# Optimization experiments

Measured on AMD Instinct MI355X. Metric: run time of the kernel, lower is better.

Reference implementation:

```python
import jax, jax.numpy as jnp
import numpy as np

HIDDEN = 4096
NUM_EXPERTS = 64
TOP_K = 2
N_TOKENS = 16384


def setup_inputs() -> dict:
    key = jax.random.key(0)
    kx, kw = jax.random.split(key)
    x = jax.random.normal(kx, (N_TOKENS, HIDDEN), dtype=jnp.float32)
    # nn.Linear(hidden, num_experts, bias=False) weight: [num_experts, hidden]
    gate_w = jax.random.normal(kw, (NUM_EXPERTS, HIDDEN), dtype=jnp.float32) * (HIDDEN ** -0.5)
    return {"x": x, "gate_w": gate_w}


def reference(x, gate_w):
    # logits: [N, num_experts]
    logits = jnp.einsum("nh,eh->ne", x, gate_w)
    topk_vals, topk_idx = jax.lax.top_k(logits, TOP_K)  # [N, k]
    topk_gates = jax.nn.softmax(topk_vals, axis=-1)
    return topk_gates, topk_idx
```

## Files before the change

kernel.cpp:

```cpp
#include <hip/hip_runtime.h>

#define NTOK 16384
#define HID  4096
#define NEXP 64
#define BM   64
#define BK   64
#define NSTEPS (HID / BK)

typedef _Float16 f16;
typedef f16  f16x4 __attribute__((ext_vector_type(4)));
typedef f16  f16x8 __attribute__((ext_vector_type(8)));
typedef float f32x4 __attribute__((ext_vector_type(4)));

__device__ __forceinline__ int swz_base(int row, int unit) {
    return row * 64 + ((unit ^ (row & 7)) << 3);
}

__global__ __launch_bounds__(512)
void topk_gate_kernel(const float* __restrict__ x,
                      const float* __restrict__ w,
                      float* __restrict__ out) {
    __shared__ __align__(16) f16 Ah[BM * BK];
    __shared__ __align__(16) f16 Al[BM * BK];
    __shared__ __align__(16) f16 Bh[NEXP * BK];
    __shared__ __align__(16) f16 Bl[NEXP * BK];
    __shared__ float red[2][BM][4];

    const int t    = threadIdx.x;
    const int blk  = blockIdx.x;
    const int lane = t & 63;
    const int wid  = t >> 6;
    const int wm   = wid & 3;
    const int wn   = wid >> 2;

    const bool isB   = (t >= 256);
    const int  tt    = t & 255;
    const int  srow  = tt >> 2;
    const int  sq    = (tt & 3) * 4;
    const float scale = isB ? 64.0f : 1.0f;
    const float* src = isB ? (w + (size_t)srow * HID + sq * 4)
                           : (x + ((size_t)blk * BM + srow) * HID + sq * 4);
    f16* dstH = isB ? Bh : Ah;
    f16* dstL = isB ? Bl : Al;

    f32x4 acc0 = {0.f, 0.f, 0.f, 0.f};
    f32x4 acc1 = {0.f, 0.f, 0.f, 0.f};

    const int col = lane & 15;
    const int grp = lane >> 4;

    float4 cur[4];
    #pragma unroll
    for (int i = 0; i < 4; ++i)
        cur[i] = *(const float4*)(src + 0 * BK + i * 4);

    for (int s = 0; s < NSTEPS; ++s) {
        const int sn = (s + 1 < NSTEPS) ? (s + 1) : s;
        float4 nxt[4];
        #pragma unroll
        for (int i = 0; i < 4; ++i)
            nxt[i] = *(const float4*)(src + (size_t)sn * BK + i * 4);

        __syncthreads();

        #pragma unroll
        for (int i = 0; i < 4; ++i) {
            float4 v = cur[i];
            float sx = v.x * scale, sy = v.y * scale, sz = v.z * scale, sw = v.w * scale;
            f16 hx = (f16)sx, hy = (f16)sy, hz = (f16)sz, hw = (f16)sw;
            f16 lx = (f16)(sx - (float)hx);
            f16 ly = (f16)(sy - (float)hy);
            f16 lz = (f16)(sz - (float)hz);
            f16 lw = (f16)(sw - (float)hw);
            int q   = sq + i;
            int off = swz_base(srow, q >> 1) + (q & 1) * 4;
            *(f16x4*)&dstH[off] = (f16x4){hx, hy, hz, hw};
            *(f16x4*)&dstL[off] = (f16x4){lx, ly, lz, lw};
        }
        __syncthreads();

        const int arow  = wm * 16 + col;
        const int brow0 = wn * 32 + col;
        const int brow1 = brow0 + 16;
        #pragma unroll
        for (int s2 = 0; s2 < 2; ++s2) {
            int u = s2 * 4 + grp;
            f16x8 ah  = *(const f16x8*)&Ah[swz_base(arow,  u)];
            f16x8 al  = *(const f16x8*)&Al[swz_base(arow,  u)];
            f16x8 b0h = *(const f16x8*)&Bh[swz_base(brow0, u)];
            f16x8 b0l = *(const f16x8*)&Bl[swz_base(brow0, u)];
            f16x8 b1h = *(const f16x8*)&Bh[swz_base(brow1, u)];
            f16x8 b1l = *(const f16x8*)&Bl[swz_base(brow1, u)];
            acc0 = __builtin_amdgcn_mfma_f32_16x16x32_f16(ah, b0h, acc0, 0, 0, 0);
            acc0 = __builtin_amdgcn_mfma_f32_16x16x32_f16(ah, b0l, acc0, 0, 0, 0);
            acc0 = __builtin_amdgcn_mfma_f32_16x16x32_f16(al, b0h, acc0, 0, 0, 0);
            acc1 = __builtin_amdgcn_mfma_f32_16x16x32_f16(ah, b1h, acc1, 0, 0, 0);
            acc1 = __builtin_amdgcn_mfma_f32_16x16x32_f16(ah, b1l, acc1, 0, 0, 0);
            acc1 = __builtin_amdgcn_mfma_f32_16x16x32_f16(al, b1h, acc1, 0, 0, 0);
        }

        #pragma unroll
        for (int i = 0; i < 4; ++i) cur[i] = nxt[i];
    }

    #pragma unroll
    for (int r = 0; r < 4; ++r) {
        float va = acc0[r], vb = acc1[r];
        int   ia = wn * 32 + col, ib = ia + 16;
        float v0, v1; int i0, i1;
        if (va >= vb) { v0 = va; i0 = ia; v1 = vb; i1 = ib; }
        else          { v0 = vb; i0 = ib; v1 = va; i1 = ia; }
        #pragma unroll
        for (int m = 1; m <= 8; m <<= 1) {
            float ov0 = __shfl_xor(v0, m, 64);
            int   oi0 = __shfl_xor(i0, m, 64);
            float ov1 = __shfl_xor(v1, m, 64);
            int   oi1 = __shfl_xor(i1, m, 64);
            bool ob = (ov0 > v0) || (ov0 == v0 && oi0 < i0);
            if (ob) {
                bool k2 = (v0 > ov1) || (v0 == ov1 && i0 < oi1);
                v1 = k2 ? v0 : ov1; i1 = k2 ? i0 : oi1;
                v0 = ov0; i0 = oi0;
            } else {
                bool k2 = (ov0 > v1) || (ov0 == v1 && oi0 < i1);
                v1 = k2 ? ov0 : v1; i1 = k2 ? oi0 : i1;
            }
        }
        if (col == 0) {
            int tl = wm * 16 + grp * 4 + r;
            red[wn][tl][0] = v0; red[wn][tl][1] = (float)i0;
            red[wn][tl][2] = v1; red[wn][tl][3] = (float)i1;
        }
    }
    __syncthreads();

    if (t < BM) {
        float a0 = red[0][t][0]; int ai0 = (int)red[0][t][1];
        float a1 = red[0][t][2]; int ai1 = (int)red[0][t][3];
        float b0 = red[1][t][0]; int bi0 = (int)red[1][t][1];
        float b1 = red[1][t][2]; int bi1 = (int)red[1][t][3];
        float v0, v1; int i0, i1;
        bool bb = (b0 > a0) || (b0 == a0 && bi0 < ai0);
        if (bb) {
            v0 = b0; i0 = bi0;
            bool k2 = (a0 > b1) || (a0 == b1 && ai0 < bi1);
            v1 = k2 ? a0 : b1; i1 = k2 ? ai0 : bi1;
        } else {
            v0 = a0; i0 = ai0;
            bool k2 = (b0 > a1) || (b0 == a1 && bi0 < ai1);
            v1 = k2 ? b0 : a1; i1 = k2 ? bi0 : ai1;
        }
        float d  = (v1 - v0) * (1.0f / 64.0f);
        float e  = expf(d);
        float g0 = 1.0f / (1.0f + e);
        float g1 = e / (1.0f + e);

        int tok = blk * BM + t;
        out[(size_t)tok * 2 + 0] = g0;
        out[(size_t)tok * 2 + 1] = g1;
        out[(size_t)NTOK * 2 + (size_t)tok * 2 + 0] = (float)i0;
        out[(size_t)NTOK * 2 + (size_t)tok * 2 + 1] = (float)i1;
    }
}

extern "C" void kernel_launch(void* const* d_in, const int* in_sizes, int n_in,
                              void* d_out, int out_size, void* d_ws, size_t ws_size,
                              hipStream_t stream) {
    const float* x = (const float*)d_in[0];
    const float* w = (const float*)d_in[1];
    float* out = (float*)d_out;
    (void)in_sizes; (void)n_in; (void)out_size; (void)d_ws; (void)ws_size;

    dim3 grid(NTOK / BM);
    dim3 block(512);
    topk_gate_kernel<<<grid, block, 0, stream>>>(x, w, out);
}
```

Before: 64.25 us.

## Prepack gate weights into MFMA fragment layout and double-buffer x tiles

Adds a pre-pass kernel that converts the gate weights once per call into hi/lo fp16 planes laid out in MFMA B-fragment order inside the workspace. The main kernel then loads B straight from global memory into registers instead of converting it into shared memory in every block and every K step. The token tile drops to 32 rows with 8 waves each owning 16 experts, the x tile is double-buffered in shared memory so there is one barrier per step, and the top-2 merge now runs over four wave groups. The cost is a second kernel launch, and all blocks re-read the packed weights from L2.

```diff
diff --git a/kernel.cpp b/kernel.cpp
--- a/kernel.cpp
+++ b/kernel.cpp
@@ -3,113 +3,128 @@
 #define NTOK 16384
 #define HID  4096
 #define NEXP 64
-#define BM   64
+#define BM   32
 #define BK   64
 #define NSTEPS (HID / BK)
+#define PLANE  (NEXP * HID)
 
 typedef _Float16 f16;
 typedef f16  f16x4 __attribute__((ext_vector_type(4)));
 typedef f16  f16x8 __attribute__((ext_vector_type(8)));
 typedef float f32x4 __attribute__((ext_vector_type(4)));
 
-__device__ __forceinline__ int swz_base(int row, int unit) {
-    return row * 64 + ((unit ^ (row & 7)) << 3);
+__device__ __forceinline__ int swz(int row, int unit16) {
+    return row * 64 + ((unit16 ^ (row & 7)) << 3);
 }
 
-__global__ __launch_bounds__(512)
+__global__ __launch_bounds__(256)
+void pack_w_kernel(const float* __restrict__ w, f16* __restrict__ wp) {
+    int tid = blockIdx.x * 256 + threadIdx.x;
+    int e = tid >> 9;
+    int k = (tid & 511) << 3;
+    const float* src = w + (size_t)e * HID + k;
+    float4 v0 = *(const float4*)(src);
+    float4 v1 = *(const float4*)(src + 4);
+    float sv[8] = {v0.x, v0.y, v0.z, v0.w, v1.x, v1.y, v1.z, v1.w};
+    f16x8 hi, lo;
+    #pragma unroll
+    for (int j = 0; j < 8; ++j) {
+        float s = sv[j] * 64.0f;
+        f16 h = (f16)s;
+        hi[j] = h;
+        lo[j] = (f16)(s - (float)h);
+    }
+    int ks   = k >> 5;
+    int g    = e >> 4;
+    int lane = ((k >> 3) & 3) * 16 + (e & 15);
+    size_t dst = ((size_t)(ks * 4 + g) * 64 + lane) * 8;
+    *(f16x8*)&wp[dst]         = hi;
+    *(f16x8*)&wp[PLANE + dst] = lo;
+}
+
+__global__ __launch_bounds__(512, 4)
 void topk_gate_kernel(const float* __restrict__ x,
-                      const float* __restrict__ w,
+                      const f16* __restrict__ wp,
                       float* __restrict__ out) {
-    __shared__ __align__(16) f16 Ah[BM * BK];
-    __shared__ __align__(16) f16 Al[BM * BK];
-    __shared__ __align__(16) f16 Bh[NEXP * BK];
-    __shared__ __align__(16) f16 Bl[NEXP * BK];
-    __shared__ float red[2][BM][4];
+    __shared__ __align__(16) f16 Ah[2][BM * BK];
+    __shared__ __align__(16) f16 Al[2][BM * BK];
+    __shared__ float red[4][BM][4];
 
     const int t    = threadIdx.x;
     const int blk  = blockIdx.x;
     const int lane = t & 63;
     const int wid  = t >> 6;
-    const int wm   = wid & 3;
-    const int wn   = wid >> 2;
+    const int wm   = wid & 1;
+    const int wn   = wid >> 1;
+    const int col  = lane & 15;
+    const int grp  = lane >> 4;
 
-    const bool isB   = (t >= 256);
-    const int  tt    = t & 255;
-    const int  srow  = tt >> 2;
-    const int  sq    = (tt & 3) * 4;
-    const float scale = isB ? 64.0f : 1.0f;
-    const float* src = isB ? (w + (size_t)srow * HID + sq * 4)
-                           : (x + ((size_t)blk * BM + srow) * HID + sq * 4);
-    f16* dstH = isB ? Bh : Ah;
-    f16* dstL = isB ? Bl : Al;
+    const int srow = t >> 4;
+    const int sq4  = t & 15;
+    const float* asrc = x + ((size_t)blk * BM + srow) * HID + sq4 * 4;
+    const int aoff = swz(srow, sq4 >> 1) + (sq4 & 1) * 4;
 
-    f32x4 acc0 = {0.f, 0.f, 0.f, 0.f};
-    f32x4 acc1 = {0.f, 0.f, 0.f, 0.f};
+    const f16* bp = wp + ((size_t)(wn * 64 + lane)) * 8;
 
-    const int col = lane & 15;
-    const int grp = lane >> 4;
+    f32x4 acc = {0.f, 0.f, 0.f, 0.f};
+    const int arow = wm * 16 + col;
 
-    float4 cur[4];
-    #pragma unroll
-    for (int i = 0; i < 4; ++i)
-        cur[i] = *(const float4*)(src + 0 * BK + i * 4);
+    float4 a_cur = *(const float4*)(asrc);
+    {
+        float4 v = a_cur;
+        f16 hx=(f16)v.x, hy=(f16)v.y, hz=(f16)v.z, hw=(f16)v.w;
+        *(f16x4*)&Ah[0][aoff] = (f16x4){hx,hy,hz,hw};
+        *(f16x4*)&Al[0][aoff] = (f16x4){(f16)(v.x-(float)hx),(f16)(v.y-(float)hy),
+                                        (f16)(v.z-(float)hz),(f16)(v.w-(float)hw)};
+    }
+    float4 a_nxt = *(const float4*)(asrc + BK);
+    f16x8 bh0c = *(const f16x8*)(bp + 0);
+    f16x8 bl0c = *(const f16x8*)(bp + PLANE + 0);
+    f16x8 bh1c = *(const f16x8*)(bp + 2048);
+    f16x8 bl1c = *(const f16x8*)(bp + PLANE + 2048);
+    __syncthreads();
 
     for (int s = 0; s < NSTEPS; ++s) {
+        const int buf = s & 1;
         const int sn = (s + 1 < NSTEPS) ? (s + 1) : s;
-        float4 nxt[4];
-        #pragma unroll
-        for (int i = 0; i < 4; ++i)
-            nxt[i] = *(const float4*)(src + (size_t)sn * BK + i * 4);
+        const size_t bo = (size_t)sn * 4096;
+        f16x8 bh0n = *(const f16x8*)(bp + bo);
+        f16x8 bl0n = *(const f16x8*)(bp + PLANE + bo);
+        f16x8 bh1n = *(const f16x8*)(bp + bo + 2048);
+        f16x8 bl1n = *(const f16x8*)(bp + PLANE + bo + 2048);
+        float4 a_n2 = (s + 2 < NSTEPS) ? *(const float4*)(asrc + (size_t)(s + 2) * BK)
+                                       : a_nxt;
 
-        __syncthreads();
+        {
+            f16x8 ah = *(const f16x8*)&Ah[buf][swz(arow, grp)];
+            f16x8 al = *(const f16x8*)&Al[buf][swz(arow, grp)];
+            acc = __builtin_amdgcn_mfma_f32_16x16x32_f16(ah, bh0c, acc, 0, 0, 0);
+            acc = __builtin_amdgcn_mfma_f32_16x16x32_f16(ah, bl0c, acc, 0, 0, 0);
+            acc = __builtin_amdgcn_mfma_f32_16x16x32_f16(al, bh0c, acc, 0, 0, 0);
+            ah = *(const f16x8*)&Ah[buf][swz(arow, 4 + grp)];
+            al = *(const f16x8*)&Al[buf][swz(arow, 4 + grp)];
+            acc = __builtin_amdgcn_mfma_f32_16x16x32_f16(ah, bh1c, acc, 0, 0, 0);
+            acc = __builtin_amdgcn_mfma_f32_16x16x32_f16(ah, bl1c, acc, 0, 0, 0);
+            acc = __builtin_amdgcn_mfma_f32_16x16x32_f16(al, bh1c, acc, 0, 0, 0);
+        }
 
-        #pragma unroll
-        for (int i = 0; i < 4; ++i) {
-            float4 v = cur[i];
-            float sx = v.x * scale, sy = v.y * scale, sz = v.z * scale, sw = v.w * scale;
-            f16 hx = (f16)sx, hy = (f16)sy, hz = (f16)sz, hw = (f16)sw;
-            f16 lx = (f16)(sx - (float)hx);
-            f16 ly = (f16)(sy - (float)hy);
-            f16 lz = (f16)(sz - (float)hz);
-            f16 lw = (f16)(sw - (float)hw);
-            int q   = sq + i;
-            int off = swz_base(srow, q >> 1) + (q & 1) * 4;
-            *(f16x4*)&dstH[off] = (f16x4){hx, hy, hz, hw};
-            *(f16x4*)&dstL[off] = (f16x4){lx, ly, lz, lw};
+        if (s + 1 < NSTEPS) {
+            float4 v = a_nxt;
+            f16 hx=(f16)v.x, hy=(f16)v.y, hz=(f16)v.z, hw=(f16)v.w;
+            *(f16x4*)&Ah[buf ^ 1][aoff] = (f16x4){hx,hy,hz,hw};
+            *(f16x4*)&Al[buf ^ 1][aoff] = (f16x4){(f16)(v.x-(float)hx),(f16)(v.y-(float)hy),
+                                                  (f16)(v.z-(float)hz),(f16)(v.w-(float)hw)};
         }
         __syncthreads();
 
-        const int arow  = wm * 16 + col;
-        const int brow0 = wn * 32 + col;
-        const int brow1 = brow0 + 16;
-        #pragma unroll
-        for (int s2 = 0; s2 < 2; ++s2) {
-            int u = s2 * 4 + grp;
-            f16x8 ah  = *(const f16x8*)&Ah[swz_base(arow,  u)];
-            f16x8 al  = *(const f16x8*)&Al[swz_base(arow,  u)];
-            f16x8 b0h = *(const f16x8*)&Bh[swz_base(brow0, u)];
-            f16x8 b0l = *(const f16x8*)&Bl[swz_base(brow0, u)];
-            f16x8 b1h = *(const f16x8*)&Bh[swz_base(brow1, u)];
-            f16x8 b1l = *(const f16x8*)&Bl[swz_base(brow1, u)];
-            acc0 = __builtin_amdgcn_mfma_f32_16x16x32_f16(ah, b0h, acc0, 0, 0, 0);
-            acc0 = __builtin_amdgcn_mfma_f32_16x16x32_f16(ah, b0l, acc0, 0, 0, 0);
-            acc0 = __builtin_amdgcn_mfma_f32_16x16x32_f16(al, b0h, acc0, 0, 0, 0);
-            acc1 = __builtin_amdgcn_mfma_f32_16x16x32_f16(ah, b1h, acc1, 0, 0, 0);
-            acc1 = __builtin_amdgcn_mfma_f32_16x16x32_f16(ah, b1l, acc1, 0, 0, 0);
-            acc1 = __builtin_amdgcn_mfma_f32_16x16x32_f16(al, b1h, acc1, 0, 0, 0);
-        }
-
-        #pragma unroll
-        for (int i = 0; i < 4; ++i) cur[i] = nxt[i];
+        a_nxt = a_n2;
+        bh0c = bh0n; bl0c = bl0n; bh1c = bh1n; bl1c = bl1n;
     }
 
     #pragma unroll
     for (int r = 0; r < 4; ++r) {
-        float va = acc0[r], vb = acc1[r];
-        int   ia = wn * 32 + col, ib = ia + 16;
-        float v0, v1; int i0, i1;
-        if (va >= vb) { v0 = va; i0 = ia; v1 = vb; i1 = ib; }
-        else          { v0 = vb; i0 = ib; v1 = va; i1 = ia; }
+        float v0 = acc[r]; int i0 = wn * 16 + col;
+        float v1 = -INFINITY; int i1 = 0x7fffffff;
         #pragma unroll
         for (int m = 1; m <= 8; m <<= 1) {
             float ov0 = __shfl_xor(v0, m, 64);
@@ -135,20 +150,21 @@
     __syncthreads();
 
     if (t < BM) {
-        float a0 = red[0][t][0]; int ai0 = (int)red[0][t][1];
-        float a1 = red[0][t][2]; int ai1 = (int)red[0][t][3];
-        float b0 = red[1][t][0]; int bi0 = (int)red[1][t][1];
-        float b1 = red[1][t][2]; int bi1 = (int)red[1][t][3];
-        float v0, v1; int i0, i1;
-        bool bb = (b0 > a0) || (b0 == a0 && bi0 < ai0);
-        if (bb) {
-            v0 = b0; i0 = bi0;
-            bool k2 = (a0 > b1) || (a0 == b1 && ai0 < bi1);
-            v1 = k2 ? a0 : b1; i1 = k2 ? ai0 : bi1;
-        } else {
-            v0 = a0; i0 = ai0;
-            bool k2 = (b0 > a1) || (b0 == a1 && bi0 < ai1);
-            v1 = k2 ? b0 : a1; i1 = k2 ? bi0 : ai1;
+        float v0 = red[0][t][0]; int i0 = (int)red[0][t][1];
+        float v1 = red[0][t][2]; int i1 = (int)red[0][t][3];
+        #pragma unroll
+        for (int g = 1; g < 4; ++g) {
+            float b0 = red[g][t][0]; int bi0 = (int)red[g][t][1];
+            float b1 = red[g][t][2]; int bi1 = (int)red[g][t][3];
+            bool bb = (b0 > v0) || (b0 == v0 && bi0 < i0);
+            if (bb) {
+                bool k2 = (v0 > b1) || (v0 == b1 && i0 < bi1);
+                float nv1 = k2 ? v0 : b1; int ni1 = k2 ? i0 : bi1;
+                v0 = b0; i0 = bi0; v1 = nv1; i1 = ni1;
+            } else {
+                bool k2 = (b0 > v1) || (b0 == v1 && bi0 < i1);
+                v1 = k2 ? b0 : v1; i1 = k2 ? bi0 : i1;
+            }
         }
         float d  = (v1 - v0) * (1.0f / 64.0f);
         float e  = expf(d);
@@ -169,9 +185,9 @@
     const float* x = (const float*)d_in[0];
     const float* w = (const float*)d_in[1];
     float* out = (float*)d_out;
-    (void)in_sizes; (void)n_in; (void)out_size; (void)d_ws; (void)ws_size;
+    f16* wp = (f16*)d_ws;
+    (void)in_sizes; (void)n_in; (void)out_size; (void)ws_size;
 
-    dim3 grid(NTOK / BM);
-    dim3 block(512);
-    topk_gate_kernel<<<grid, block, 0, stream>>>(x, w, out);
+    pack_w_kernel<<<dim3(128), dim3(256), 0, stream>>>(w, wp);
+    topk_gate_kernel<<<dim3(NTOK / BM), dim3(512), 0, stream>>>(x, wp, out);
 }
```

Result: slower. 78.78 us (+22.6%).
